# Kernel optimization log

Hardware: AMD Instinct MI355X
Metric: run time of the kernel (lower is better)

Reference implementation:

```python
import jax, jax.numpy as jnp
import numpy as np

SEQ_LEN = 4096
INPUT_SIZE = 1024
OUTPUT_SIZE = 1024


def _xavier(key, shape):
    n = shape[0]
    lim = 1.0 / (n ** 0.5)
    return jax.random.uniform(key, shape, minval=-lim, maxval=lim, dtype=jnp.float32)


def setup_inputs() -> dict:
    key = jax.random.key(0)
    kx, kk, kv, kq = jax.random.split(key, 4)
    X = jax.random.normal(kx, (SEQ_LEN, INPUT_SIZE), dtype=jnp.float32)
    Wk = _xavier(kk, (INPUT_SIZE, OUTPUT_SIZE))
    Wv = _xavier(kv, (INPUT_SIZE, OUTPUT_SIZE))
    Wq = _xavier(kq, (INPUT_SIZE, OUTPUT_SIZE))
    return {"X": X, "Wk": Wk, "Wv": Wv, "Wq": Wq}


def reference(X, Wk, Wv, Wq):
    # Faithful to original: scores = K @ Q^T (note K first, no 1/sqrt(d) scaling)
    K = X @ Wk  # (S, D)
    V = X @ Wv  # (S, D)
    Q = X @ Wq  # (S, D)
    scores = jnp.einsum('sd,td->st', K, Q)  # (S, S) == K @ Q^T
    attn = jax.nn.softmax(scores, axis=-1) @ V  # (S, D)
    return attn
```

## Files before the change

### kernel.cpp

```cpp
#include <hip/hip_runtime.h>
#include <hip/hip_fp16.h>
#include <cstdint>

#define SEQ 4096
#define DIM 1024

typedef _Float16 f16x8 __attribute__((ext_vector_type(8)));
typedef float f32x16 __attribute__((ext_vector_type(16)));
typedef __attribute__((address_space(1))) void as1_void;
typedef __attribute__((address_space(3))) void as3_void;

__device__ __forceinline__ ushort f2h(float f) {
  _Float16 h = (_Float16)f;
  return __builtin_bit_cast(ushort, h);
}

__global__ void convert_all_kernel(const float* __restrict__ X, const float* __restrict__ Wk,
                                   const float* __restrict__ Wv, const float* __restrict__ Wq,
                                   ushort* __restrict__ Xh, ushort* __restrict__ Wt) {
  const int z = blockIdx.z;
  const int tx = threadIdx.x, ty = threadIdx.y;
  if (z == 3) {
    const int bid = blockIdx.y * 32 + blockIdx.x;
    const int t = ty * 32 + tx;
#pragma unroll
    for (int k = 0; k < 4; k++) {
      int i = bid * 1024 + k * 256 + t;
      float4 v = reinterpret_cast<const float4*>(X)[i];
      ushort4 o = { f2h(v.x), f2h(v.y), f2h(v.z), f2h(v.w) };
      reinterpret_cast<ushort4*>(Xh)[i] = o;
    }
    return;
  }
  __shared__ float tile[32][33];
  const float* W = (z == 0) ? Wk : (z == 1) ? Wv : Wq;
  int n0 = blockIdx.x * 32, k0 = blockIdx.y * 32;
#pragma unroll
  for (int r = 0; r < 4; r++) {
    int k = ty + r * 8;
    tile[k][tx] = W[(size_t)(k0 + k) * DIM + n0 + tx];
  }
  __syncthreads();
  ushort* out = Wt + (size_t)z * DIM * DIM;
#pragma unroll
  for (int r = 0; r < 4; r++) {
    int n = ty + r * 8;
    out[(size_t)(n0 + n) * DIM + k0 + tx] = f2h(tile[tx][n]);
  }
}

template <bool F16_OUT>
__device__ __forceinline__ void gemm_tile(const ushort* __restrict__ A,
                                          const ushort* __restrict__ B,
                                          void* __restrict__ C,
                                          int N, int K, int m0, int n0,
                                          int kt0, int ktend) {
  constexpr int BK = 64;
  __shared__ __align__(16) ushort As[128 * BK];
  __shared__ __align__(16) ushort Bs[128 * BK];
  const int tid = threadIdx.x;
  const int wave = tid >> 6, lane = tid & 63;
  const int l31 = lane & 31, khalf = lane >> 5;
  const int wm = (wave & 1) * 64, wn = (wave >> 1) * 64;

  const int srow = tid >> 3;
  const int skey = ((srow & 7) ^ ((srow >> 3) & 3));
  const int sce = (((tid & 7) ^ skey) * 8);
  const int rk = (l31 & 7) ^ ((l31 >> 3) & 3);

  f32x16 acc[2][2];
#pragma unroll
  for (int i = 0; i < 2; i++)
#pragma unroll
    for (int j = 0; j < 2; j++)
#pragma unroll
      for (int r = 0; r < 16; r++) acc[i][j][r] = 0.f;

  for (int kt = kt0; kt < ktend; kt += BK) {
    __syncthreads();
#pragma unroll
    for (int q = 0; q < 4; q++) {
      const ushort* ga = A + (size_t)(m0 + srow + q * 32) * K + kt + sce;
      __builtin_amdgcn_global_load_lds((const as1_void*)ga,
                                       (as3_void*)&As[wave * 512 + q * 2048], 16, 0, 0);
    }
#pragma unroll
    for (int q = 0; q < 4; q++) {
      const ushort* gb = B + (size_t)(n0 + srow + q * 32) * K + kt + sce;
      __builtin_amdgcn_global_load_lds((const as1_void*)gb,
                                       (as3_void*)&Bs[wave * 512 + q * 2048], 16, 0, 0);
    }
    __syncthreads();
#pragma unroll
    for (int ks = 0; ks < 4; ks++) {
      f16x8 af[2], bfr[2];
      const int ck = (ks * 2 + khalf);
#pragma unroll
      for (int i = 0; i < 2; i++)
        af[i] = *reinterpret_cast<const f16x8*>(
            &As[(wm + i * 32 + l31) * BK + ((ck ^ rk) * 8)]);
#pragma unroll
      for (int j = 0; j < 2; j++)
        bfr[j] = *reinterpret_cast<const f16x8*>(
            &Bs[(wn + j * 32 + l31) * BK + ((ck ^ rk) * 8)]);
#pragma unroll
      for (int i = 0; i < 2; i++)
#pragma unroll
        for (int j = 0; j < 2; j++)
          acc[i][j] = __builtin_amdgcn_mfma_f32_32x32x16_f16(af[i], bfr[j], acc[i][j], 0, 0, 0);
    }
  }

#pragma unroll
  for (int i = 0; i < 2; i++)
#pragma unroll
    for (int j = 0; j < 2; j++)
#pragma unroll
      for (int r = 0; r < 16; r++) {
        int row = m0 + wm + i * 32 + (r & 3) + 8 * (r >> 2) + 4 * khalf;
        int col = n0 + wn + j * 32 + l31;
        if (F16_OUT)
          reinterpret_cast<ushort*>(C)[(size_t)row * N + col] = f2h(acc[i][j][r]);
        else
          reinterpret_cast<float*>(C)[(size_t)row * N + col] = acc[i][j][r];
      }
}

__global__ __launch_bounds__(256) void proj_kernel(const ushort* __restrict__ Xh,
                                                   const ushort* __restrict__ Wt,
                                                   ushort* __restrict__ Kh,
                                                   ushort* __restrict__ Qh,
                                                   ushort* __restrict__ Vt) {
  const int z = blockIdx.z;
  const ushort* A;
  const ushort* B;
  ushort* C;
  int N, m0, n0;
  if (z < 2) {
    A = Xh;
    B = Wt + (size_t)(z == 0 ? 0 : 2) * DIM * DIM;
    C = (z == 0) ? Kh : Qh;
    N = DIM;
    m0 = (blockIdx.x >> 3) * 128;
    n0 = (blockIdx.x & 7) * 128;
  } else {
    A = Wt + (size_t)DIM * DIM;
    B = Xh;
    C = Vt;
    N = SEQ;
    m0 = (blockIdx.x >> 5) * 128;
    n0 = (blockIdx.x & 31) * 128;
  }
  gemm_tile<true>(A, B, C, N, DIM, m0, n0, 0, DIM);
}

__global__ __launch_bounds__(256) void score_kernel(const ushort* __restrict__ Kh,
                                                    const ushort* __restrict__ Qh,
                                                    ushort* __restrict__ S) {
  const int f = blockIdx.x;
  const int xcd = f & 7;
  const int r = f >> 3;
  const int t = xcd * 128 + r;
  const int st = t >> 6, within = t & 63;
  const int sx = within & 7, sy = within >> 3;
  const int tx = (st & 3) * 8 + sx;
  const int ty = (st >> 2) * 8 + sy;
  gemm_tile<true>(Kh, Qh, S, SEQ, DIM, ty * 128, tx * 128, 0, DIM);
}

__global__ __launch_bounds__(256) void out_splitk_kernel(const ushort* __restrict__ P,
                                                         const ushort* __restrict__ Vt,
                                                         ushort* __restrict__ Part) {
  const int f = blockIdx.x;
  const int z = f >> 8;
  const int q = f & 255;
  const int xcd = q & 7;
  const int r = q >> 3;
  const int t = xcd * 32 + r;
  const int tx = t & 7, ty = t >> 3;
  ushort* C = Part + (size_t)z * SEQ * DIM;
  gemm_tile<true>(P, Vt, C, DIM, SEQ, ty * 128, tx * 128,
                  z * (SEQ / 4), (z + 1) * (SEQ / 4));
}

__global__ void reduce4_kernel(const ushort* __restrict__ Part, float* __restrict__ out, int n8) {
  int i = blockIdx.x * blockDim.x + threadIdx.x;
  if (i >= n8) return;
  const f16x8* p0 = reinterpret_cast<const f16x8*>(Part);
  const f16x8* p1 = p0 + n8;
  const f16x8* p2 = p1 + n8;
  const f16x8* p3 = p2 + n8;
  f16x8 a = p0[i], b = p1[i], c = p2[i], d = p3[i];
  float4 lo, hi;
  lo.x = (float)a[0] + (float)b[0] + (float)c[0] + (float)d[0];
  lo.y = (float)a[1] + (float)b[1] + (float)c[1] + (float)d[1];
  lo.z = (float)a[2] + (float)b[2] + (float)c[2] + (float)d[2];
  lo.w = (float)a[3] + (float)b[3] + (float)c[3] + (float)d[3];
  hi.x = (float)a[4] + (float)b[4] + (float)c[4] + (float)d[4];
  hi.y = (float)a[5] + (float)b[5] + (float)c[5] + (float)d[5];
  hi.z = (float)a[6] + (float)b[6] + (float)c[6] + (float)d[6];
  hi.w = (float)a[7] + (float)b[7] + (float)c[7] + (float)d[7];
  reinterpret_cast<float4*>(out)[i * 2] = lo;
  reinterpret_cast<float4*>(out)[i * 2 + 1] = hi;
}

__global__ __launch_bounds__(256) void softmax_kernel(const ushort* __restrict__ S,
                                                      ushort* __restrict__ P) {
  const int wave = threadIdx.x >> 6, lane = threadIdx.x & 63;
  const int row = blockIdx.x * 4 + wave;
  const ushort* s = S + (size_t)row * SEQ;
  float v[64];
#pragma unroll
  for (int i = 0; i < 8; i++) {
    f16x8 h = reinterpret_cast<const f16x8*>(s)[i * 64 + lane];
#pragma unroll
    for (int j = 0; j < 8; j++) v[i * 8 + j] = (float)h[j];
  }
  float m = v[0];
#pragma unroll
  for (int j = 1; j < 64; j++) m = fmaxf(m, v[j]);
#pragma unroll
  for (int o = 32; o > 0; o >>= 1) m = fmaxf(m, __shfl_xor(m, o, 64));
  float sum = 0.f;
#pragma unroll
  for (int j = 0; j < 64; j++) {
    v[j] = __expf(v[j] - m);
    sum += v[j];
  }
#pragma unroll
  for (int o = 32; o > 0; o >>= 1) sum += __shfl_xor(sum, o, 64);
  float inv = 1.0f / sum;
  ushort* p = P + (size_t)row * SEQ;
#pragma unroll
  for (int i = 0; i < 8; i++) {
    f16x8 h;
#pragma unroll
    for (int j = 0; j < 8; j++) h[j] = (_Float16)(v[i * 8 + j] * inv);
    reinterpret_cast<f16x8*>(p)[i * 64 + lane] = h;
  }
}

extern "C" void kernel_launch(void* const* d_in, const int* in_sizes, int n_in,
                              void* d_out, int out_size, void* d_ws, size_t ws_size,
                              hipStream_t stream) {
  const float* X = (const float*)d_in[0];
  const float* Wk = (const float*)d_in[1];
  const float* Wv = (const float*)d_in[2];
  const float* Wq = (const float*)d_in[3];

  char* ws = (char*)d_ws;
  size_t off = 0;
  ushort* Xh = (ushort*)(ws + off); off += (size_t)SEQ * DIM * 2;
  ushort* Wt = (ushort*)(ws + off); off += (size_t)3 * DIM * DIM * 2;
  ushort* Kh = (ushort*)(ws + off); off += (size_t)SEQ * DIM * 2;
  ushort* Qh = (ushort*)(ws + off); off += (size_t)SEQ * DIM * 2;
  ushort* Vt = (ushort*)(ws + off); off += (size_t)SEQ * DIM * 2;
  ushort* S = (ushort*)(ws + off);  off += (size_t)SEQ * SEQ * 2;
  ushort* P = (ushort*)(ws + off);  off += (size_t)SEQ * SEQ * 2;

  ushort* Part = S;

  convert_all_kernel<<<dim3(32, 32, 4), dim3(32, 8), 0, stream>>>(X, Wk, Wv, Wq, Xh, Wt);
  proj_kernel<<<dim3(256, 1, 3), 256, 0, stream>>>(Xh, Wt, Kh, Qh, Vt);
  score_kernel<<<1024, 256, 0, stream>>>(Kh, Qh, S);
  softmax_kernel<<<1024, 256, 0, stream>>>(S, P);
  out_splitk_kernel<<<1024, 256, 0, stream>>>(P, Vt, Part);
  reduce4_kernel<<<SEQ * DIM / 8 / 256, 256, 0, stream>>>(Part, (float*)d_out, SEQ * DIM / 8);
}
```

Measured before the change: 211.0 us.

## Use 256x256 GEMM tiles with 512 threads and double-buffered LDS prefetch

Replaces the 128x128, 256-thread GEMM tile with a 256x256 tile computed by 8 waves, each holding a 64x128 accumulator block. The LDS buffers for A and B are doubled so the next K-slice is loaded while the current one feeds the MFMAs, leaving one barrier per iteration. The projection, score and split-K output grids and their XCD-aware block remapping are resized to match. The aim is more data reuse per tile and hiding global-load latency. In exchange, about 128KB of LDS per block allows only one block per CU, and there are fewer blocks overall.

Result: no change. 210.2 us (-0.4%).

```diff
diff --git a/kernel.cpp b/kernel.cpp
--- a/kernel.cpp
+++ b/kernel.cpp
@@ -49,64 +49,75 @@
   }
 }
 
-template <bool F16_OUT>
-__device__ __forceinline__ void gemm_tile(const ushort* __restrict__ A,
-                                          const ushort* __restrict__ B,
-                                          void* __restrict__ C,
-                                          int N, int K, int m0, int n0,
-                                          int kt0, int ktend) {
+__device__ __forceinline__ void gemm512(const ushort* __restrict__ A,
+                                        const ushort* __restrict__ B,
+                                        ushort* __restrict__ C,
+                                        int N, int K, int m0, int n0,
+                                        int kt0, int ktend) {
   constexpr int BK = 64;
-  __shared__ __align__(16) ushort As[128 * BK];
-  __shared__ __align__(16) ushort Bs[128 * BK];
+  __shared__ __align__(16) ushort As[2][256 * BK];
+  __shared__ __align__(16) ushort Bs[2][256 * BK];
   const int tid = threadIdx.x;
   const int wave = tid >> 6, lane = tid & 63;
   const int l31 = lane & 31, khalf = lane >> 5;
-  const int wm = (wave & 1) * 64, wn = (wave >> 1) * 64;
+  const int wm = (wave & 3) * 64, wn = (wave >> 2) * 128;
 
   const int srow = tid >> 3;
-  const int skey = ((srow & 7) ^ ((srow >> 3) & 3));
+  const int skey = (srow & 7) ^ ((srow >> 3) & 3);
   const int sce = (((tid & 7) ^ skey) * 8);
   const int rk = (l31 & 7) ^ ((l31 >> 3) & 3);
 
-  f32x16 acc[2][2];
+  const ushort* Abase = A + (size_t)(m0 + srow) * K + sce;
+  const ushort* Bbase = B + (size_t)(n0 + srow) * K + sce;
+
+  f32x16 acc[2][4];
 #pragma unroll
   for (int i = 0; i < 2; i++)
 #pragma unroll
-    for (int j = 0; j < 2; j++)
+    for (int j = 0; j < 4; j++)
 #pragma unroll
       for (int r = 0; r < 16; r++) acc[i][j][r] = 0.f;
 
-  for (int kt = kt0; kt < ktend; kt += BK) {
+  const int niter = (ktend - kt0) / BK;
+
+#pragma unroll
+  for (int q = 0; q < 4; q++) {
+    __builtin_amdgcn_global_load_lds((const as1_void*)(Abase + (size_t)q * 64 * K + kt0),
+                                     (as3_void*)&As[0][wave * 512 + q * 4096], 16, 0, 0);
+    __builtin_amdgcn_global_load_lds((const as1_void*)(Bbase + (size_t)q * 64 * K + kt0),
+                                     (as3_void*)&Bs[0][wave * 512 + q * 4096], 16, 0, 0);
+  }
+
+  for (int it = 0; it < niter; ++it) {
     __syncthreads();
-#pragma unroll
-    for (int q = 0; q < 4; q++) {
-      const ushort* ga = A + (size_t)(m0 + srow + q * 32) * K + kt + sce;
-      __builtin_amdgcn_global_load_lds((const as1_void*)ga,
-                                       (as3_void*)&As[wave * 512 + q * 2048], 16, 0, 0);
+    if (it + 1 < niter) {
+      const int kt = kt0 + (it + 1) * BK;
+      const int nb = (it + 1) & 1;
+#pragma unroll
+      for (int q = 0; q < 4; q++) {
+        __builtin_amdgcn_global_load_lds((const as1_void*)(Abase + (size_t)q * 64 * K + kt),
+                                         (as3_void*)&As[nb][wave * 512 + q * 4096], 16, 0, 0);
+        __builtin_amdgcn_global_load_lds((const as1_void*)(Bbase + (size_t)q * 64 * K + kt),
+                                         (as3_void*)&Bs[nb][wave * 512 + q * 4096], 16, 0, 0);
+      }
     }
-#pragma unroll
-    for (int q = 0; q < 4; q++) {
-      const ushort* gb = B + (size_t)(n0 + srow + q * 32) * K + kt + sce;
-      __builtin_amdgcn_global_load_lds((const as1_void*)gb,
-                                       (as3_void*)&Bs[wave * 512 + q * 2048], 16, 0, 0);
-    }
-    __syncthreads();
+    const int cb = it & 1;
 #pragma unroll
     for (int ks = 0; ks < 4; ks++) {
-      f16x8 af[2], bfr[2];
+      f16x8 af[2], bfr[4];
       const int ck = (ks * 2 + khalf);
 #pragma unroll
       for (int i = 0; i < 2; i++)
         af[i] = *reinterpret_cast<const f16x8*>(
-            &As[(wm + i * 32 + l31) * BK + ((ck ^ rk) * 8)]);
-#pragma unroll
-      for (int j = 0; j < 2; j++)
+            &As[cb][(wm + i * 32 + l31) * BK + ((ck ^ rk) * 8)]);
+#pragma unroll
+      for (int j = 0; j < 4; j++)
         bfr[j] = *reinterpret_cast<const f16x8*>(
-            &Bs[(wn + j * 32 + l31) * BK + ((ck ^ rk) * 8)]);
+            &Bs[cb][(wn + j * 32 + l31) * BK + ((ck ^ rk) * 8)]);
 #pragma unroll
       for (int i = 0; i < 2; i++)
 #pragma unroll
-        for (int j = 0; j < 2; j++)
+        for (int j = 0; j < 4; j++)
           acc[i][j] = __builtin_amdgcn_mfma_f32_32x32x16_f16(af[i], bfr[j], acc[i][j], 0, 0, 0);
     }
   }
@@ -114,73 +125,59 @@
 #pragma unroll
   for (int i = 0; i < 2; i++)
 #pragma unroll
-    for (int j = 0; j < 2; j++)
+    for (int j = 0; j < 4; j++)
 #pragma unroll
       for (int r = 0; r < 16; r++) {
         int row = m0 + wm + i * 32 + (r & 3) + 8 * (r >> 2) + 4 * khalf;
         int col = n0 + wn + j * 32 + l31;
-        if (F16_OUT)
-          reinterpret_cast<ushort*>(C)[(size_t)row * N + col] = f2h(acc[i][j][r]);
-        else
-          reinterpret_cast<float*>(C)[(size_t)row * N + col] = acc[i][j][r];
+        C[(size_t)row * N + col] = f2h(acc[i][j][r]);
       }
 }
 
-__global__ __launch_bounds__(256) void proj_kernel(const ushort* __restrict__ Xh,
-                                                   const ushort* __restrict__ Wt,
-                                                   ushort* __restrict__ Kh,
-                                                   ushort* __restrict__ Qh,
-                                                   ushort* __restrict__ Vt) {
+__global__ __launch_bounds__(512, 2) void proj_kernel(const ushort* __restrict__ Xh,
+                                                      const ushort* __restrict__ Wt,
+                                                      ushort* __restrict__ Kh,
+                                                      ushort* __restrict__ Qh,
+                                                      ushort* __restrict__ Vt) {
   const int z = blockIdx.z;
-  const ushort* A;
-  const ushort* B;
-  ushort* C;
-  int N, m0, n0;
+  const int bx = blockIdx.x;
   if (z < 2) {
-    A = Xh;
-    B = Wt + (size_t)(z == 0 ? 0 : 2) * DIM * DIM;
-    C = (z == 0) ? Kh : Qh;
-    N = DIM;
-    m0 = (blockIdx.x >> 3) * 128;
-    n0 = (blockIdx.x & 7) * 128;
+    const ushort* B = Wt + (size_t)(z == 0 ? 0 : 2) * DIM * DIM;
+    ushort* C = (z == 0) ? Kh : Qh;
+    gemm512(Xh, B, C, DIM, DIM, (bx >> 2) * 256, (bx & 3) * 256, 0, DIM);
   } else {
-    A = Wt + (size_t)DIM * DIM;
-    B = Xh;
-    C = Vt;
-    N = SEQ;
-    m0 = (blockIdx.x >> 5) * 128;
-    n0 = (blockIdx.x & 31) * 128;
-  }
-  gemm_tile<true>(A, B, C, N, DIM, m0, n0, 0, DIM);
-}
-
-__global__ __launch_bounds__(256) void score_kernel(const ushort* __restrict__ Kh,
-                                                    const ushort* __restrict__ Qh,
-                                                    ushort* __restrict__ S) {
+    gemm512(Wt + (size_t)DIM * DIM, Xh, Vt, SEQ, DIM,
+            (bx >> 4) * 256, (bx & 15) * 256, 0, DIM);
+  }
+}
+
+__global__ __launch_bounds__(512, 2) void score_kernel(const ushort* __restrict__ Kh,
+                                                       const ushort* __restrict__ Qh,
+                                                       ushort* __restrict__ S) {
   const int f = blockIdx.x;
   const int xcd = f & 7;
   const int r = f >> 3;
-  const int t = xcd * 128 + r;
-  const int st = t >> 6, within = t & 63;
-  const int sx = within & 7, sy = within >> 3;
-  const int tx = (st & 3) * 8 + sx;
-  const int ty = (st >> 2) * 8 + sy;
-  gemm_tile<true>(Kh, Qh, S, SEQ, DIM, ty * 128, tx * 128, 0, DIM);
-}
-
-__global__ __launch_bounds__(256) void out_splitk_kernel(const ushort* __restrict__ P,
-                                                         const ushort* __restrict__ Vt,
-                                                         ushort* __restrict__ Part) {
+  const int g = xcd * 2 + (r >> 4);
+  const int w = r & 15;
+  const int sx = w & 3, sy = w >> 2;
+  const int tx = (g & 3) * 4 + sx;
+  const int ty = (g >> 2) * 4 + sy;
+  gemm512(Kh, Qh, S, SEQ, DIM, ty * 256, tx * 256, 0, DIM);
+}
+
+__global__ __launch_bounds__(512, 2) void out_splitk_kernel(const ushort* __restrict__ P,
+                                                            const ushort* __restrict__ Vt,
+                                                            ushort* __restrict__ Part) {
   const int f = blockIdx.x;
-  const int z = f >> 8;
-  const int q = f & 255;
-  const int xcd = q & 7;
-  const int r = q >> 3;
-  const int t = xcd * 32 + r;
-  const int tx = t & 7, ty = t >> 3;
+  const int xcd = f & 7;
+  const int r = f >> 3;
+  const int z = r >> 3;
+  const int u = r & 7;
+  const int t = xcd * 8 + u;
+  const int ty = t >> 2, tx = t & 3;
   ushort* C = Part + (size_t)z * SEQ * DIM;
-  gemm_tile<true>(P, Vt, C, DIM, SEQ, ty * 128, tx * 128,
-                  z * (SEQ / 4), (z + 1) * (SEQ / 4));
+  gemm512(P, Vt, C, DIM, SEQ, ty * 256, tx * 256,
+          z * (SEQ / 4), (z + 1) * (SEQ / 4));
 }
 
 __global__ void reduce4_kernel(const ushort* __restrict__ Part, float* __restrict__ out, int n8) {
@@ -261,9 +258,9 @@
   ushort* Part = S;
 
   convert_all_kernel<<<dim3(32, 32, 4), dim3(32, 8), 0, stream>>>(X, Wk, Wv, Wq, Xh, Wt);
-  proj_kernel<<<dim3(256, 1, 3), 256, 0, stream>>>(Xh, Wt, Kh, Qh, Vt);
-  score_kernel<<<1024, 256, 0, stream>>>(Kh, Qh, S);
+  proj_kernel<<<dim3(64, 1, 3), 512, 0, stream>>>(Xh, Wt, Kh, Qh, Vt);
+  score_kernel<<<256, 512, 0, stream>>>(Kh, Qh, S);
   softmax_kernel<<<1024, 256, 0, stream>>>(S, P);
-  out_splitk_kernel<<<1024, 256, 0, stream>>>(P, Vt, Part);
+  out_splitk_kernel<<<256, 512, 0, stream>>>(P, Vt, Part);
   reduce4_kernel<<<SEQ * DIM / 8 / 256, 256, 0, stream>>>(Part, (float*)d_out, SEQ * DIM / 8);
 }
```
